# Optimization experiments

Hardware: AMD Instinct MI355X
Metric: run time of the kernel (lower is better)

## Reference

```python
import jax, jax.numpy as jnp
import numpy as np

DIM = 256
NUM_HEADS = 4
WINDOW = 64
EPS = 1e-6


def setup_inputs() -> dict:
    key = jax.random.key(0)
    ks = jax.random.split(key, 12)
    d = DIM
    s = 0.02
    return {
        "x": jax.random.normal(ks[0], (4, 2049, d), dtype=jnp.float32),
        "norm1_w": jnp.ones((d,), jnp.float32),
        "in_proj_w": jax.random.normal(ks[1], (3 * d, d), jnp.float32) * s,
        "in_proj_b": jnp.zeros((3 * d,), jnp.float32),
        "out_proj_w": jax.random.normal(ks[2], (d, d), jnp.float32) * s,
        "out_proj_b": jnp.zeros((d,), jnp.float32),
        "norm2_w": jnp.ones((d,), jnp.float32),
        "w1": jax.random.normal(ks[3], (2 * d, d), jnp.float32) * s,
        "b1": jnp.zeros((2 * d,), jnp.float32),
        "w2": jax.random.normal(ks[4], (d, 2 * d), jnp.float32) * s,
        "b2": jnp.zeros((d,), jnp.float32),
    }


def _rmsnorm(x, w):
    r = jax.lax.rsqrt(jnp.mean(x * x, axis=-1, keepdims=True) + EPS)
    return x * r * w


def _factorized_mask(size):
    # global token 0 attends/attended everywhere; others banded within WINDOW
    idx = jnp.arange(size)
    band = jnp.abs(idx[:, None] - idx[None, :]) <= WINDOW
    allowed = band | (idx[:, None] == 0) | (idx[None, :] == 0)
    return jnp.where(allowed, 0.0, -jnp.inf).astype(jnp.float32)


def reference(x, norm1_w, in_proj_w, in_proj_b, out_proj_w, out_proj_b,
              norm2_w, w1, b1, w2, b2):
    B, S, D = x.shape
    H = NUM_HEADS
    dh = D // H
    residual = x
    h = _rmsnorm(x, norm1_w)
    # fused qkv projection (torch MHA in_proj): [B,S,3D]
    qkv = h @ in_proj_w.T + in_proj_b
    q, k, v = jnp.split(qkv, 3, axis=-1)
    q = q.reshape(B, S, H, dh).transpose(0, 2, 1, 3)  # [B,H,S,dh]
    k = k.reshape(B, S, H, dh).transpose(0, 2, 1, 3)
    v = v.reshape(B, S, H, dh).transpose(0, 2, 1, 3)
    scores = jnp.einsum("bhqd,bhkd->bhqk", q, k) / jnp.sqrt(jnp.float32(dh))
    scores = scores + _factorized_mask(S)  # additive -inf mask
    attn = jax.nn.softmax(scores, axis=-1)
    ctx = jnp.einsum("bhqk,bhkd->bhqd", attn, v)
    ctx = ctx.transpose(0, 2, 1, 3).reshape(B, S, D)
    attn_out = ctx @ out_proj_w.T + out_proj_b
    x1 = residual + attn_out
    h2 = _rmsnorm(x1, norm2_w)
    ffn = jax.nn.gelu(h2 @ w1.T + b1, approximate=False) @ w2.T + b2
    return x1 + ffn
```

## Files before the change

kernel.cpp:

```cpp
#include <hip/hip_runtime.h>
#include <hip/hip_bf16.h>
#include <math.h>

#define BATCH 4
#define SEQ 2049
#define DIMD 256
#define WIN 64
#define M_ROWS (BATCH * SEQ)
#define M_PAD 8320

#define QBLK 33
#define NKB 10
#define PSTR 168
#define VGUARD 64
#define VW 2256
#define QKSTR 512

#define NSPLIT 33
#define VT_F4 288768

typedef __attribute__((ext_vector_type(8))) short short8;
typedef __attribute__((ext_vector_type(4))) float f32x4;
typedef __hip_bfloat16 bf16;

__device__ __forceinline__ float b2f(short u) {
    union { unsigned int i; float f; } c;
    c.i = ((unsigned int)(unsigned short)u) << 16;
    return c.f;
}
__device__ __forceinline__ short f2b(float f) {
    bf16 h = __float2bfloat16(f);
    return *reinterpret_cast<short*>(&h);
}

__global__ __launch_bounds__(256) void prep_kernel(
        const float* __restrict__ wq, const float* __restrict__ wo,
        const float* __restrict__ w1, const float* __restrict__ w2,
        bf16* __restrict__ oq, bf16* __restrict__ oo,
        bf16* __restrict__ o1, bf16* __restrict__ o2,
        const float* __restrict__ x, const float* __restrict__ nw,
        bf16* __restrict__ h, float4* __restrict__ vTz) {
    const int bi = blockIdx.x, tid = threadIdx.x;
    if (bi < 2048) {
        int i = bi * 256 + tid;
        if (i < 196608)      oq[i]          = __float2bfloat16(wq[i]);
        else if (i < 262144) oo[i - 196608] = __float2bfloat16(wo[i - 196608]);
        else if (i < 393216) o1[i - 262144] = __float2bfloat16(w1[i - 262144]);
        else                 o2[i - 393216] = __float2bfloat16(w2[i - 393216]);
        return;
    }
    if (bi >= 4097) {
        int zi = (bi - 4097) * 256 + tid;
        #pragma unroll
        for (int it = 0; it < 3; it++) {
            int idx = zi + it * 512 * 256;
            if (idx < VT_F4) vTz[idx] = (float4){0.f, 0.f, 0.f, 0.f};
        }
        return;
    }
    int wid = tid >> 6, lane = tid & 63;
    int row = (bi - 2048) * 4 + wid;
    if (row >= M_ROWS) return;
    const float4 v = reinterpret_cast<const float4*>(x + (size_t)row * DIMD)[lane];
    float ss = v.x * v.x + v.y * v.y + v.z * v.z + v.w * v.w;
    #pragma unroll
    for (int o = 1; o < 64; o <<= 1) ss += __shfl_xor(ss, o, 64);
    float r = rsqrtf(ss * (1.0f / DIMD) + 1e-6f);
    const float4 wv = reinterpret_cast<const float4*>(nw)[lane];
    bf16* hp = h + (size_t)row * DIMD + lane * 4;
    hp[0] = __float2bfloat16(v.x * r * wv.x);
    hp[1] = __float2bfloat16(v.y * r * wv.y);
    hp[2] = __float2bfloat16(v.z * r * wv.z);
    hp[3] = __float2bfloat16(v.w * r * wv.w);
}

__global__ __launch_bounds__(256) void gemm_qkv(
        const bf16* __restrict__ A, const bf16* __restrict__ B,
        const float* __restrict__ bias, bf16* __restrict__ qk, short* __restrict__ vT) {
    __shared__ __align__(16) short lA[8 * 128 * 8];
    __shared__ __align__(16) short lB[8 * 128 * 8];
    const int tid = threadIdx.x, lane = tid & 63, wid = tid >> 6;
    const int m0 = blockIdx.x * 128;
    const int n0 = blockIdx.y * 128;
    const int wr = wid >> 1, wc = wid & 1;
    const int r = lane & 15, g = lane >> 4;
    const int K = 256;

    f32x4 acc[4][4];
    #pragma unroll
    for (int i = 0; i < 4; i++)
        #pragma unroll
        for (int j = 0; j < 4; j++) acc[i][j] = (f32x4){0.f, 0.f, 0.f, 0.f};

    for (int k0 = 0; k0 < K; k0 += 64) {
        #pragma unroll
        for (int it = 0; it < 4; ++it) {
            int c = it * 256 + tid;
            int kc = c >> 7, row = c & 127;
            __builtin_amdgcn_global_load_lds(
                (const __attribute__((address_space(1))) void*)(A + (size_t)(m0 + row) * K + k0 + kc * 8),
                (__attribute__((address_space(3))) void*)&lA[c * 8], 16, 0, 0);
        }
        #pragma unroll
        for (int it = 0; it < 4; ++it) {
            int c = it * 256 + tid;
            int kc = c >> 7, row = c & 127;
            __builtin_amdgcn_global_load_lds(
                (const __attribute__((address_space(1))) void*)(B + (size_t)(n0 + row) * K + k0 + kc * 8),
                (__attribute__((address_space(3))) void*)&lB[c * 8], 16, 0, 0);
        }
        __syncthreads();
        #pragma unroll
        for (int kk = 0; kk < 2; kk++) {
            short8 a[4], b[4];
            #pragma unroll
            for (int mi = 0; mi < 4; mi++)
                a[mi] = *reinterpret_cast<const short8*>(&lA[((kk * 4 + g) * 128 + wr * 64 + mi * 16 + r) * 8]);
            #pragma unroll
            for (int ni = 0; ni < 4; ni++)
                b[ni] = *reinterpret_cast<const short8*>(&lB[((kk * 4 + g) * 128 + wc * 64 + ni * 16 + r) * 8]);
            #pragma unroll
            for (int mi = 0; mi < 4; mi++)
                #pragma unroll
                for (int ni = 0; ni < 4; ni++)
                    acc[mi][ni] = __builtin_amdgcn_mfma_f32_16x16x32_bf16(a[mi], b[ni], acc[mi][ni], 0, 0, 0);
        }
        __syncthreads();
    }

    const int c0 = lane & 15, r0 = (lane >> 4) * 4;
    const bool isV = (n0 >= 512);
    #pragma unroll
    for (int mi = 0; mi < 4; mi++) {
        #pragma unroll
        for (int ni = 0; ni < 4; ni++) {
            int col = n0 + wc * 64 + ni * 16 + c0;
            float bv = bias[col];
            #pragma unroll
            for (int j = 0; j < 4; j++) {
                int row = m0 + wr * 64 + mi * 16 + r0 + j;
                if (row < M_ROWS) {
                    float v = acc[mi][ni][j] + bv;
                    if (!isV) {
                        qk[(size_t)row * QKSTR + col] = __float2bfloat16(v);
                    } else {
                        int dcol = col - 512, hh = dcol >> 6, d = dcol & 63;
                        int bb = row >> 11;
                        int js = row - bb * SEQ;
                        if (js < 0) { bb--; js += SEQ; }
                        vT[((size_t)((bb * 4 + hh) * 64 + d)) * VW + VGUARD + js] = f2b(v);
                    }
                }
            }
        }
    }
}

template<int MODE, int BN>
__global__ __launch_bounds__(256) void gemm_lds(
        const bf16* __restrict__ A, const bf16* __restrict__ B,
        const float* __restrict__ bias, const float* __restrict__ resid,
        void* __restrict__ C, int M, int N, int K) {
    constexpr int FN = BN / 32;
    __shared__ __align__(16) short lA[8 * 128 * 8];
    __shared__ __align__(16) short lB[8 * BN * 8];
    const int tid = threadIdx.x, lane = tid & 63, wid = tid >> 6;
    const int m0 = blockIdx.x * 128;
    const int n0 = blockIdx.y * BN;
    const int wr = wid >> 1, wc = wid & 1;
    const int r = lane & 15, g = lane >> 4;

    f32x4 acc[4][FN];
    #pragma unroll
    for (int i = 0; i < 4; i++)
        #pragma unroll
        for (int j = 0; j < FN; j++) acc[i][j] = (f32x4){0.f, 0.f, 0.f, 0.f};

    for (int k0 = 0; k0 < K; k0 += 64) {
        #pragma unroll
        for (int it = 0; it < 4; ++it) {
            int c = it * 256 + tid;
            int kc = c >> 7, row = c & 127;
            __builtin_amdgcn_global_load_lds(
                (const __attribute__((address_space(1))) void*)(A + (size_t)(m0 + row) * K + k0 + kc * 8),
                (__attribute__((address_space(3))) void*)&lA[c * 8], 16, 0, 0);
        }
        #pragma unroll
        for (int it = 0; it < BN / 32; ++it) {
            int c = it * 256 + tid;
            int kc = c / BN, row = c % BN;
            __builtin_amdgcn_global_load_lds(
                (const __attribute__((address_space(1))) void*)(B + (size_t)(n0 + row) * K + k0 + kc * 8),
                (__attribute__((address_space(3))) void*)&lB[c * 8], 16, 0, 0);
        }
        __syncthreads();
        #pragma unroll
        for (int kk = 0; kk < 2; kk++) {
            short8 a[4], b[FN];
            #pragma unroll
            for (int mi = 0; mi < 4; mi++)
                a[mi] = *reinterpret_cast<const short8*>(&lA[((kk * 4 + g) * 128 + wr * 64 + mi * 16 + r) * 8]);
            #pragma unroll
            for (int ni = 0; ni < FN; ni++)
                b[ni] = *reinterpret_cast<const short8*>(&lB[((kk * 4 + g) * BN + wc * (BN / 2) + ni * 16 + r) * 8]);
            #pragma unroll
            for (int mi = 0; mi < 4; mi++)
                #pragma unroll
                for (int ni = 0; ni < FN; ni++)
                    acc[mi][ni] = __builtin_amdgcn_mfma_f32_16x16x32_bf16(a[mi], b[ni], acc[mi][ni], 0, 0, 0);
        }
        __syncthreads();
    }

    const int c0 = lane & 15, r0 = (lane >> 4) * 4;
    #pragma unroll
    for (int mi = 0; mi < 4; mi++) {
        #pragma unroll
        for (int ni = 0; ni < FN; ni++) {
            int col = n0 + wc * (BN / 2) + ni * 16 + c0;
            float bv = bias[col];
            #pragma unroll
            for (int j = 0; j < 4; j++) {
                int row = m0 + wr * 64 + mi * 16 + r0 + j;
                if (row < M) {
                    float v = acc[mi][ni][j] + bv;
                    if (MODE == 2) v = 0.5f * v * (1.0f + erff(v * 0.70710678118654752f));
                    if (MODE == 1) {
                        v += resid[(size_t)row * N + col];
                        reinterpret_cast<float*>(C)[(size_t)row * N + col] = v;
                    } else {
                        reinterpret_cast<bf16*>(C)[(size_t)row * N + col] = __float2bfloat16(v);
                    }
                }
            }
        }
    }
}

__global__ __launch_bounds__(256) void gemm_or(
        const bf16* __restrict__ A, const bf16* __restrict__ B,
        const float* __restrict__ bias, const float* __restrict__ resid,
        const float* __restrict__ nw,
        float* __restrict__ x1, bf16* __restrict__ h2) {
    __shared__ __align__(16) short lA[8 * 32 * 8];
    __shared__ __align__(16) short lB[8 * 256 * 8];
    __shared__ float osq[4][32];
    const int tid = threadIdx.x, lane = tid & 63, wid = tid >> 6;
    const int m0 = blockIdx.x * 32;
    const int wc = wid;
    const int r = lane & 15, g = lane >> 4;
    const int K = 256;

    f32x4 acc[2][4];
    #pragma unroll
    for (int i = 0; i < 2; i++)
        #pragma unroll
        for (int j = 0; j < 4; j++) acc[i][j] = (f32x4){0.f, 0.f, 0.f, 0.f};

    for (int k0 = 0; k0 < K; k0 += 64) {
        {
            int c = tid;
            int kc = c >> 5, row = c & 31;
            __builtin_amdgcn_global_load_lds(
                (const __attribute__((address_space(1))) void*)(A + (size_t)(m0 + row) * K + k0 + kc * 8),
                (__attribute__((address_space(3))) void*)&lA[c * 8], 16, 0, 0);
        }
        #pragma unroll
        for (int it = 0; it < 8; ++it) {
            int c = it * 256 + tid;
            int kc = c >> 8, row = c & 255;
            __builtin_amdgcn_global_load_lds(
                (const __attribute__((address_space(1))) void*)(B + (size_t)row * K + k0 + kc * 8),
                (__attribute__((address_space(3))) void*)&lB[c * 8], 16, 0, 0);
        }
        __syncthreads();
        #pragma unroll
        for (int kk = 0; kk < 2; kk++) {
            short8 a[2], b[4];
            #pragma unroll
            for (int mi = 0; mi < 2; mi++)
                a[mi] = *reinterpret_cast<const short8*>(&lA[((kk * 4 + g) * 32 + mi * 16 + r) * 8]);
            #pragma unroll
            for (int ni = 0; ni < 4; ni++)
                b[ni] = *reinterpret_cast<const short8*>(&lB[((kk * 4 + g) * 256 + wc * 64 + ni * 16 + r) * 8]);
            #pragma unroll
            for (int mi = 0; mi < 2; mi++)
                #pragma unroll
                for (int ni = 0; ni < 4; ni++)
                    acc[mi][ni] = __builtin_amdgcn_mfma_f32_16x16x32_bf16(a[mi], b[ni], acc[mi][ni], 0, 0, 0);
        }
        __syncthreads();
    }

    const int c0 = lane & 15, r0 = (lane >> 4) * 4;
    float ssq[2][4];
    #pragma unroll
    for (int mi = 0; mi < 2; mi++) {
        #pragma unroll
        for (int j = 0; j < 4; j++) {
            int row = m0 + mi * 16 + r0 + j;
            float s = 0.f;
            if (row < M_ROWS) {
                #pragma unroll
                for (int ni = 0; ni < 4; ni++) {
                    int col = wc * 64 + ni * 16 + c0;
                    float v = acc[mi][ni][j] + bias[col] + resid[(size_t)row * 256 + col];
                    acc[mi][ni][j] = v;
                    x1[(size_t)row * 256 + col] = v;
                    s += v * v;
                }
            }
            ssq[mi][j] = s;
        }
    }
    #pragma unroll
    for (int o = 1; o < 16; o <<= 1) {
        #pragma unroll
        for (int mi = 0; mi < 2; mi++)
            #pragma unroll
            for (int j = 0; j < 4; j++) ssq[mi][j] += __shfl_xor(ssq[mi][j], o, 64);
    }
    if (c0 == 0) {
        #pragma unroll
        for (int mi = 0; mi < 2; mi++)
            #pragma unroll
            for (int j = 0; j < 4; j++) osq[wc][mi * 16 + r0 + j] = ssq[mi][j];
    }
    __syncthreads();
    #pragma unroll
    for (int mi = 0; mi < 2; mi++) {
        #pragma unroll
        for (int j = 0; j < 4; j++) {
            int lr = mi * 16 + r0 + j;
            int row = m0 + lr;
            if (row < M_ROWS) {
                float tot = osq[0][lr] + osq[1][lr] + osq[2][lr] + osq[3][lr];
                float rs = rsqrtf(tot * (1.0f / 256.0f) + 1e-6f);
                #pragma unroll
                for (int ni = 0; ni < 4; ni++) {
                    int col = wc * 64 + ni * 16 + c0;
                    h2[(size_t)row * 256 + col] = __float2bfloat16(acc[mi][ni][j] * rs * nw[col]);
                }
            }
        }
    }
}

__global__ __launch_bounds__(256) void attn_partial(const bf16* __restrict__ qk,
                                                    const short* __restrict__ vT,
                                                    float* __restrict__ part) {
    __shared__ float q_s[64];
    __shared__ float p_s[64];
    __shared__ float meta[2];
    __shared__ float osum[4][64];
    const int tid = threadIdx.x;
    const int bh = blockIdx.x / NSPLIT, s = blockIdx.x % NSPLIT;
    const int b = bh >> 2, h = bh & 3;
    const size_t base = (size_t)b * SEQ;
    const int j0 = s * 64;
    const int lane = tid & 63, wid = tid >> 6;

    if (tid < 64) q_s[tid] = __bfloat162float(qk[base * QKSTR + h * 64 + tid]);
    __syncthreads();

    if (wid == 0) {
        int j = j0 + lane;
        float sc = -1e30f;
        if (j < SEQ) {
            const short8* kp = reinterpret_cast<const short8*>(
                reinterpret_cast<const short*>(qk) + (base + j) * QKSTR + 256 + h * 64);
            float acc = 0.f;
            #pragma unroll
            for (int d8 = 0; d8 < 8; ++d8) {
                short8 kv = kp[d8];
                #pragma unroll
                for (int e = 0; e < 8; ++e) acc += q_s[d8 * 8 + e] * b2f(kv[e]);
            }
            sc = acc * 0.125f;
        }
        float mx = sc;
        #pragma unroll
        for (int o = 1; o < 64; o <<= 1) mx = fmaxf(mx, __shfl_xor(mx, o, 64));
        float p = (j < SEQ) ? expf(sc - mx) : 0.f;
        p_s[lane] = p;
        float l = p;
        #pragma unroll
        for (int o = 1; o < 64; o <<= 1) l += __shfl_xor(l, o, 64);
        if (lane == 0) { meta[0] = mx; meta[1] = l; }
    }
    __syncthreads();

    const short* vrow = vT + ((size_t)bh * 64 + lane) * VW + VGUARD + j0;
    float oa = 0.f;
    #pragma unroll
    for (int i0 = 0; i0 < 16; i0++) {
        int i = wid + i0 * 4;
        if (j0 + i < SEQ) oa += p_s[i] * b2f(vrow[i]);
    }
    osum[wid][lane] = oa;
    __syncthreads();
    if (wid == 0) {
        float o = osum[0][lane] + osum[1][lane] + osum[2][lane] + osum[3][lane];
        float* pp = part + (size_t)(bh * NSPLIT + s) * 66;
        pp[lane] = o;
        if (lane == 0) { pp[64] = meta[0]; pp[65] = meta[1]; }
    }
}

__global__ __launch_bounds__(256) void attn_band_mfma(const bf16* __restrict__ qkb,
                                                      const short* __restrict__ vT,
                                                      const float* __restrict__ part,
                                                      short* __restrict__ ctx) {
    __shared__ short p_lds[4][16][PSTR];
    const short* qk = reinterpret_cast<const short*>(qkb);
    const int tid = threadIdx.x, lane = tid & 63, wid = tid >> 6;
    const int qb = blockIdx.x % QBLK;
    const int bh = blockIdx.x / QBLK;
    const int b = bh >> 2, h = bh & 3;
    const size_t rbase = (size_t)b * SEQ;
    const int q0w = qb * 64 + wid * 16;
    const int jbase = q0w - 64;
    const int lrow = lane & 15;
    const int koff = (lane >> 4) * 8;
    const int c0 = lrow, r0 = (lane >> 4) * 4;

    int qrow = q0w + lrow; if (qrow > SEQ - 1) qrow = SEQ - 1;
    const short* qp = qk + (rbase + qrow) * QKSTR + h * 64;
    short8 aq0 = *reinterpret_cast<const short8*>(qp + koff);
    short8 aq1 = *reinterpret_cast<const short8*>(qp + 32 + koff);

    const short* k0p = qk + rbase * QKSTR + 256 + h * 64;
    short8 k0a = *reinterpret_cast<const short8*>(k0p + koff);
    short8 k0b = *reinterpret_cast<const short8*>(k0p + 32 + koff);
    float s0 = 0.f;
    #pragma unroll
    for (int e = 0; e < 8; e++)
        s0 += b2f(aq0[e]) * b2f(k0a[e]) + b2f(aq1[e]) * b2f(k0b[e]);
    s0 += __shfl_xor(s0, 16, 64);
    s0 += __shfl_xor(s0, 32, 64);

    f32x4 s[NKB];
    #pragma unroll
    for (int n = 0; n < NKB; n++) {
        int j = jbase + n * 16 + lrow;
        int jc = j < 0 ? 0 : (j > SEQ - 1 ? SEQ - 1 : j);
        const short* kp = qk + (rbase + jc) * QKSTR + 256 + h * 64;
        short8 bk0 = *reinterpret_cast<const short8*>(kp + koff);
        short8 bk1 = *reinterpret_cast<const short8*>(kp + 32 + koff);
        f32x4 acc = (f32x4){0.f, 0.f, 0.f, 0.f};
        acc = __builtin_amdgcn_mfma_f32_16x16x32_bf16(aq0, bk0, acc, 0, 0, 0);
        acc = __builtin_amdgcn_mfma_f32_16x16x32_bf16(aq1, bk1, acc, 0, 0, 0);
        s[n] = acc;
    }

    const float SC = 0.125f * 1.44269504088896340736f;
    const bool g1 = (jbase > 0);
    float s0q[4], m4[4];
    #pragma unroll
    for (int jj = 0; jj < 4; jj++) {
        s0q[jj] = __shfl(s0, r0 + jj, 64) * SC;
        m4[jj] = g1 ? s0q[jj] : -1e30f;
    }
    #pragma unroll
    for (int n = 0; n < NKB; n++) {
        int j = jbase + n * 16 + c0;
        bool jv = (j >= 0) && (j < SEQ);
        #pragma unroll
        for (int jj = 0; jj < 4; jj++) {
            int q = q0w + r0 + jj;
            int dd = q - j; if (dd < 0) dd = -dd;
            bool allowed = jv && (dd <= WIN || j == 0);
            float v = allowed ? s[n][jj] * SC : -1e30f;
            s[n][jj] = v;
            m4[jj] = fmaxf(m4[jj], v);
        }
    }
    #pragma unroll
    for (int o = 1; o < 16; o <<= 1) {
        #pragma unroll
        for (int jj = 0; jj < 4; jj++) m4[jj] = fmaxf(m4[jj], __shfl_xor(m4[jj], o, 64));
    }

    float p0[4], l4[4];
    #pragma unroll
    for (int jj = 0; jj < 4; jj++) {
        p0[jj] = g1 ? exp2f(s0q[jj] - m4[jj]) : 0.f;
        l4[jj] = p0[jj];
    }
    #pragma unroll
    for (int n = 0; n < NKB; n++) {
        #pragma unroll
        for (int jj = 0; jj < 4; jj++) {
            float p = exp2f(s[n][jj] - m4[jj]);
            l4[jj] += p;
            p_lds[wid][r0 + jj][n * 16 + c0] = f2b(p);
        }
    }
    #pragma unroll
    for (int o = 1; o < 16; o <<= 1) {
        #pragma unroll
        for (int jj = 0; jj < 4; jj++) l4[jj] += __shfl_xor(l4[jj], o, 64);
    }

    __syncthreads();

    f32x4 o[4];
    #pragma unroll
    for (int dn = 0; dn < 4; dn++) o[dn] = (f32x4){0.f, 0.f, 0.f, 0.f};
    #pragma unroll
    for (int ks = 0; ks < NKB / 2; ks++) {
        short8 ap = *reinterpret_cast<const short8*>(&p_lds[wid][lrow][ks * 32 + koff]);
        int cc = VGUARD + jbase + ks * 32 + koff;
        #pragma unroll
        for (int dn = 0; dn < 4; dn++) {
            short8 bv = *reinterpret_cast<const short8*>(
                vT + ((size_t)bh * 64 + dn * 16 + lrow) * VW + cc);
            o[dn] = __builtin_amdgcn_mfma_f32_16x16x32_bf16(ap, bv, o[dn], 0, 0, 0);
        }
    }

    #pragma unroll
    for (int jj = 0; jj < 4; jj++) {
        int q = q0w + r0 + jj;
        if (q >= 1 && q < SEQ) {
            float rl = 1.0f / l4[jj];
            #pragma unroll
            for (int dn = 0; dn < 4; dn++) {
                float v0 = b2f(vT[((size_t)bh * 64 + dn * 16 + c0) * VW + VGUARD]);
                float val = (o[dn][jj] + p0[jj] * v0) * rl;
                ctx[(rbase + q) * 256 + h * 64 + dn * 16 + c0] = f2b(val);
            }
        }
    }

    if (qb == 0) {
        __syncthreads();
        if (wid == 0) {
            float m = (lane < NSPLIT) ? part[(size_t)(bh * NSPLIT + lane) * 66 + 64] : -1e30f;
            #pragma unroll
            for (int o2 = 1; o2 < 64; o2 <<= 1) m = fmaxf(m, __shfl_xor(m, o2, 64));
            float L = 0.f, ov = 0.f;
            for (int sp = 0; sp < NSPLIT; sp++) {
                const float* pp = part + (size_t)(bh * NSPLIT + sp) * 66;
                float w = expf(pp[64] - m);
                L += pp[65] * w;
                ov += pp[lane] * w;
            }
            ctx[rbase * 256 + h * 64 + lane] = f2b(ov / L);
        }
    }
}

extern "C" void kernel_launch(void* const* d_in, const int* in_sizes, int n_in,
                              void* d_out, int out_size, void* d_ws, size_t ws_size,
                              hipStream_t stream) {
    const float* x         = (const float*)d_in[0];
    const float* norm1_w   = (const float*)d_in[1];
    const float* in_proj_w = (const float*)d_in[2];
    const float* in_proj_b = (const float*)d_in[3];
    const float* out_proj_w= (const float*)d_in[4];
    const float* out_proj_b= (const float*)d_in[5];
    const float* norm2_w   = (const float*)d_in[6];
    const float* w1        = (const float*)d_in[7];
    const float* b1        = (const float*)d_in[8];
    const float* w2        = (const float*)d_in[9];
    const float* b2        = (const float*)d_in[10];
    float* out = (float*)d_out;

    const int M = M_ROWS;
    char* ws = (char*)d_ws;
    size_t off = 0;
    auto take = [&](size_t bytes) {
        char* p = ws + off;
        off = (off + bytes + 255) & ~(size_t)255;
        return p;
    };
    bf16* h_bf   = (bf16*)take((size_t)M_PAD * 256 * 2);
    bf16* qk_bf  = (bf16*)take((size_t)M_PAD * QKSTR * 2);
    bf16* ctx_bf = (bf16*)take((size_t)M_PAD * 256 * 2);
    float* x1    = (float*)take((size_t)M_PAD * 256 * 4);
    bf16* h2_bf  = (bf16*)take((size_t)M_PAD * 256 * 2);
    bf16* g_bf   = (bf16*)take((size_t)M_PAD * 512 * 2);
    bf16* wq_bf  = (bf16*)take(768 * 256 * 2);
    bf16* wo_bf  = (bf16*)take(256 * 256 * 2);
    bf16* w1_bf  = (bf16*)take(512 * 256 * 2);
    bf16* w2_bf  = (bf16*)take(256 * 512 * 2);
    float* part  = (float*)take((size_t)16 * NSPLIT * 66 * 4);
    short* vT    = (short*)take((size_t)16 * 64 * VW * 2);
    (void)ws_size; (void)in_sizes; (void)n_in; (void)out_size;

    prep_kernel<<<dim3(4609), dim3(256), 0, stream>>>(
        in_proj_w, out_proj_w, w1, w2, wq_bf, wo_bf, w1_bf, w2_bf,
        x, norm1_w, h_bf, (float4*)vT);
    gemm_qkv<<<dim3(65, 6), dim3(256), 0, stream>>>(h_bf, wq_bf, in_proj_b, qk_bf, vT);
    attn_partial<<<dim3(16 * NSPLIT), dim3(256), 0, stream>>>(qk_bf, vT, part);
    attn_band_mfma<<<dim3(16 * QBLK), dim3(256), 0, stream>>>(qk_bf, vT, part, (short*)ctx_bf);
    gemm_or<<<dim3(257), dim3(256), 0, stream>>>(ctx_bf, wo_bf, out_proj_b, x, norm2_w, x1, h2_bf);
    gemm_lds<2, 128><<<dim3(65, 4), dim3(256), 0, stream>>>(h2_bf, w1_bf, b1, (const float*)nullptr,
                                                            (void*)g_bf, M, 512, 256);
    gemm_lds<1, 64><<<dim3(65, 4), dim3(256), 0, stream>>>(g_bf, w2_bf, b2, x1,
                                                           (void*)out, M, 256, 512);
}
```

Measured before the change: 127.8 us.

## Fuse attention with out-projection/RMSNorm and fuse both FFN GEMMs

Attention is restructured so each block covers 16 query rows for all 4 heads of one batch. Each block keeps its context tile in LDS and immediately applies the out-projection, residual add and RMSNorm, so the ctx buffer and the separate gemm_or launch go away. The two FFN GEMMs are fused into one kernel that computes the GELU hidden activations in 128-column chunks in LDS and accumulates the second GEMM directly, which removes the g buffer round trip and a launch. In exchange, weight fragments are read straight from global memory without LDS staging, and the attention grid becomes smaller (516 blocks), which may lower efficiency.

```diff
diff --git a/kernel.cpp b/kernel.cpp
--- a/kernel.cpp
+++ b/kernel.cpp
@@ -9,9 +9,11 @@
 #define M_ROWS (BATCH * SEQ)
 #define M_PAD 8320
 
-#define QBLK 33
+#define QT16 129
 #define NKB 10
 #define PSTR 168
+#define CSTR 264
+#define GSTR 136
 #define VGUARD 64
 #define VW 2256
 #define QKSTR 512
@@ -156,196 +158,6 @@
     }
 }
 
-template<int MODE, int BN>
-__global__ __launch_bounds__(256) void gemm_lds(
-        const bf16* __restrict__ A, const bf16* __restrict__ B,
-        const float* __restrict__ bias, const float* __restrict__ resid,
-        void* __restrict__ C, int M, int N, int K) {
-    constexpr int FN = BN / 32;
-    __shared__ __align__(16) short lA[8 * 128 * 8];
-    __shared__ __align__(16) short lB[8 * BN * 8];
-    const int tid = threadIdx.x, lane = tid & 63, wid = tid >> 6;
-    const int m0 = blockIdx.x * 128;
-    const int n0 = blockIdx.y * BN;
-    const int wr = wid >> 1, wc = wid & 1;
-    const int r = lane & 15, g = lane >> 4;
-
-    f32x4 acc[4][FN];
-    #pragma unroll
-    for (int i = 0; i < 4; i++)
-        #pragma unroll
-        for (int j = 0; j < FN; j++) acc[i][j] = (f32x4){0.f, 0.f, 0.f, 0.f};
-
-    for (int k0 = 0; k0 < K; k0 += 64) {
-        #pragma unroll
-        for (int it = 0; it < 4; ++it) {
-            int c = it * 256 + tid;
-            int kc = c >> 7, row = c & 127;
-            __builtin_amdgcn_global_load_lds(
-                (const __attribute__((address_space(1))) void*)(A + (size_t)(m0 + row) * K + k0 + kc * 8),
-                (__attribute__((address_space(3))) void*)&lA[c * 8], 16, 0, 0);
-        }
-        #pragma unroll
-        for (int it = 0; it < BN / 32; ++it) {
-            int c = it * 256 + tid;
-            int kc = c / BN, row = c % BN;
-            __builtin_amdgcn_global_load_lds(
-                (const __attribute__((address_space(1))) void*)(B + (size_t)(n0 + row) * K + k0 + kc * 8),
-                (__attribute__((address_space(3))) void*)&lB[c * 8], 16, 0, 0);
-        }
-        __syncthreads();
-        #pragma unroll
-        for (int kk = 0; kk < 2; kk++) {
-            short8 a[4], b[FN];
-            #pragma unroll
-            for (int mi = 0; mi < 4; mi++)
-                a[mi] = *reinterpret_cast<const short8*>(&lA[((kk * 4 + g) * 128 + wr * 64 + mi * 16 + r) * 8]);
-            #pragma unroll
-            for (int ni = 0; ni < FN; ni++)
-                b[ni] = *reinterpret_cast<const short8*>(&lB[((kk * 4 + g) * BN + wc * (BN / 2) + ni * 16 + r) * 8]);
-            #pragma unroll
-            for (int mi = 0; mi < 4; mi++)
-                #pragma unroll
-                for (int ni = 0; ni < FN; ni++)
-                    acc[mi][ni] = __builtin_amdgcn_mfma_f32_16x16x32_bf16(a[mi], b[ni], acc[mi][ni], 0, 0, 0);
-        }
-        __syncthreads();
-    }
-
-    const int c0 = lane & 15, r0 = (lane >> 4) * 4;
-    #pragma unroll
-    for (int mi = 0; mi < 4; mi++) {
-        #pragma unroll
-        for (int ni = 0; ni < FN; ni++) {
-            int col = n0 + wc * (BN / 2) + ni * 16 + c0;
-            float bv = bias[col];
-            #pragma unroll
-            for (int j = 0; j < 4; j++) {
-                int row = m0 + wr * 64 + mi * 16 + r0 + j;
-                if (row < M) {
-                    float v = acc[mi][ni][j] + bv;
-                    if (MODE == 2) v = 0.5f * v * (1.0f + erff(v * 0.70710678118654752f));
-                    if (MODE == 1) {
-                        v += resid[(size_t)row * N + col];
-                        reinterpret_cast<float*>(C)[(size_t)row * N + col] = v;
-                    } else {
-                        reinterpret_cast<bf16*>(C)[(size_t)row * N + col] = __float2bfloat16(v);
-                    }
-                }
-            }
-        }
-    }
-}
-
-__global__ __launch_bounds__(256) void gemm_or(
-        const bf16* __restrict__ A, const bf16* __restrict__ B,
-        const float* __restrict__ bias, const float* __restrict__ resid,
-        const float* __restrict__ nw,
-        float* __restrict__ x1, bf16* __restrict__ h2) {
-    __shared__ __align__(16) short lA[8 * 32 * 8];
-    __shared__ __align__(16) short lB[8 * 256 * 8];
-    __shared__ float osq[4][32];
-    const int tid = threadIdx.x, lane = tid & 63, wid = tid >> 6;
-    const int m0 = blockIdx.x * 32;
-    const int wc = wid;
-    const int r = lane & 15, g = lane >> 4;
-    const int K = 256;
-
-    f32x4 acc[2][4];
-    #pragma unroll
-    for (int i = 0; i < 2; i++)
-        #pragma unroll
-        for (int j = 0; j < 4; j++) acc[i][j] = (f32x4){0.f, 0.f, 0.f, 0.f};
-
-    for (int k0 = 0; k0 < K; k0 += 64) {
-        {
-            int c = tid;
-            int kc = c >> 5, row = c & 31;
-            __builtin_amdgcn_global_load_lds(
-                (const __attribute__((address_space(1))) void*)(A + (size_t)(m0 + row) * K + k0 + kc * 8),
-                (__attribute__((address_space(3))) void*)&lA[c * 8], 16, 0, 0);
-        }
-        #pragma unroll
-        for (int it = 0; it < 8; ++it) {
-            int c = it * 256 + tid;
-            int kc = c >> 8, row = c & 255;
-            __builtin_amdgcn_global_load_lds(
-                (const __attribute__((address_space(1))) void*)(B + (size_t)row * K + k0 + kc * 8),
-                (__attribute__((address_space(3))) void*)&lB[c * 8], 16, 0, 0);
-        }
-        __syncthreads();
-        #pragma unroll
-        for (int kk = 0; kk < 2; kk++) {
-            short8 a[2], b[4];
-            #pragma unroll
-            for (int mi = 0; mi < 2; mi++)
-                a[mi] = *reinterpret_cast<const short8*>(&lA[((kk * 4 + g) * 32 + mi * 16 + r) * 8]);
-            #pragma unroll
-            for (int ni = 0; ni < 4; ni++)
-                b[ni] = *reinterpret_cast<const short8*>(&lB[((kk * 4 + g) * 256 + wc * 64 + ni * 16 + r) * 8]);
-            #pragma unroll
-            for (int mi = 0; mi < 2; mi++)
-                #pragma unroll
-                for (int ni = 0; ni < 4; ni++)
-                    acc[mi][ni] = __builtin_amdgcn_mfma_f32_16x16x32_bf16(a[mi], b[ni], acc[mi][ni], 0, 0, 0);
-        }
-        __syncthreads();
-    }
-
-    const int c0 = lane & 15, r0 = (lane >> 4) * 4;
-    float ssq[2][4];
-    #pragma unroll
-    for (int mi = 0; mi < 2; mi++) {
-        #pragma unroll
-        for (int j = 0; j < 4; j++) {
-            int row = m0 + mi * 16 + r0 + j;
-            float s = 0.f;
-            if (row < M_ROWS) {
-                #pragma unroll
-                for (int ni = 0; ni < 4; ni++) {
-                    int col = wc * 64 + ni * 16 + c0;
-                    float v = acc[mi][ni][j] + bias[col] + resid[(size_t)row * 256 + col];
-                    acc[mi][ni][j] = v;
-                    x1[(size_t)row * 256 + col] = v;
-                    s += v * v;
-                }
-            }
-            ssq[mi][j] = s;
-        }
-    }
-    #pragma unroll
-    for (int o = 1; o < 16; o <<= 1) {
-        #pragma unroll
-        for (int mi = 0; mi < 2; mi++)
-            #pragma unroll
-            for (int j = 0; j < 4; j++) ssq[mi][j] += __shfl_xor(ssq[mi][j], o, 64);
-    }
-    if (c0 == 0) {
-        #pragma unroll
-        for (int mi = 0; mi < 2; mi++)
-            #pragma unroll
-            for (int j = 0; j < 4; j++) osq[wc][mi * 16 + r0 + j] = ssq[mi][j];
-    }
-    __syncthreads();
-    #pragma unroll
-    for (int mi = 0; mi < 2; mi++) {
-        #pragma unroll
-        for (int j = 0; j < 4; j++) {
-            int lr = mi * 16 + r0 + j;
-            int row = m0 + lr;
-            if (row < M_ROWS) {
-                float tot = osq[0][lr] + osq[1][lr] + osq[2][lr] + osq[3][lr];
-                float rs = rsqrtf(tot * (1.0f / 256.0f) + 1e-6f);
-                #pragma unroll
-                for (int ni = 0; ni < 4; ni++) {
-                    int col = wc * 64 + ni * 16 + c0;
-                    h2[(size_t)row * 256 + col] = __float2bfloat16(acc[mi][ni][j] * rs * nw[col]);
-                }
-            }
-        }
-    }
-}
-
 __global__ __launch_bounds__(256) void attn_partial(const bf16* __restrict__ qk,
                                                     const short* __restrict__ vT,
                                                     float* __restrict__ part) {
@@ -407,24 +219,27 @@
     }
 }
 
-__global__ __launch_bounds__(256) void attn_band_mfma(const bf16* __restrict__ qkb,
-                                                      const short* __restrict__ vT,
-                                                      const float* __restrict__ part,
-                                                      short* __restrict__ ctx) {
+__global__ __launch_bounds__(256) void attn_or(
+        const bf16* __restrict__ qkb, const short* __restrict__ vT,
+        const float* __restrict__ part, const bf16* __restrict__ wo,
+        const float* __restrict__ ob, const float* __restrict__ x,
+        const float* __restrict__ nw, float* __restrict__ x1, bf16* __restrict__ h2) {
     __shared__ short p_lds[4][16][PSTR];
+    __shared__ short ctx_lds[16][CSTR];
+    __shared__ float osq[4][16];
     const short* qk = reinterpret_cast<const short*>(qkb);
-    const int tid = threadIdx.x, lane = tid & 63, wid = tid >> 6;
-    const int qb = blockIdx.x % QBLK;
-    const int bh = blockIdx.x / QBLK;
-    const int b = bh >> 2, h = bh & 3;
+    const int tid = threadIdx.x, lane = tid & 63, h = tid >> 6;
+    const int qt = blockIdx.x % QT16;
+    const int b = blockIdx.x / QT16;
+    const int bh = b * 4 + h;
     const size_t rbase = (size_t)b * SEQ;
-    const int q0w = qb * 64 + wid * 16;
-    const int jbase = q0w - 64;
+    const int q0 = qt * 16;
+    const int jbase = q0 - 64;
     const int lrow = lane & 15;
     const int koff = (lane >> 4) * 8;
     const int c0 = lrow, r0 = (lane >> 4) * 4;
 
-    int qrow = q0w + lrow; if (qrow > SEQ - 1) qrow = SEQ - 1;
+    int qrow = q0 + lrow; if (qrow > SEQ - 1) qrow = SEQ - 1;
     const short* qp = qk + (rbase + qrow) * QKSTR + h * 64;
     short8 aq0 = *reinterpret_cast<const short8*>(qp + koff);
     short8 aq1 = *reinterpret_cast<const short8*>(qp + 32 + koff);
@@ -467,7 +282,7 @@
         bool jv = (j >= 0) && (j < SEQ);
         #pragma unroll
         for (int jj = 0; jj < 4; jj++) {
-            int q = q0w + r0 + jj;
+            int q = q0 + r0 + jj;
             int dd = q - j; if (dd < 0) dd = -dd;
             bool allowed = jv && (dd <= WIN || j == 0);
             float v = allowed ? s[n][jj] * SC : -1e30f;
@@ -493,7 +308,7 @@
         for (int jj = 0; jj < 4; jj++) {
             float p = exp2f(s[n][jj] - m4[jj]);
             l4[jj] += p;
-            p_lds[wid][r0 + jj][n * 16 + c0] = f2b(p);
+            p_lds[h][r0 + jj][n * 16 + c0] = f2b(p);
         }
     }
     #pragma unroll
@@ -502,14 +317,12 @@
         for (int jj = 0; jj < 4; jj++) l4[jj] += __shfl_xor(l4[jj], o, 64);
     }
 
-    __syncthreads();
-
     f32x4 o[4];
     #pragma unroll
     for (int dn = 0; dn < 4; dn++) o[dn] = (f32x4){0.f, 0.f, 0.f, 0.f};
     #pragma unroll
     for (int ks = 0; ks < NKB / 2; ks++) {
-        short8 ap = *reinterpret_cast<const short8*>(&p_lds[wid][lrow][ks * 32 + koff]);
+        short8 ap = *reinterpret_cast<const short8*>(&p_lds[h][lrow][ks * 32 + koff]);
         int cc = VGUARD + jbase + ks * 32 + koff;
         #pragma unroll
         for (int dn = 0; dn < 4; dn++) {
@@ -521,32 +334,182 @@
 
     #pragma unroll
     for (int jj = 0; jj < 4; jj++) {
-        int q = q0w + r0 + jj;
-        if (q >= 1 && q < SEQ) {
-            float rl = 1.0f / l4[jj];
-            #pragma unroll
-            for (int dn = 0; dn < 4; dn++) {
-                float v0 = b2f(vT[((size_t)bh * 64 + dn * 16 + c0) * VW + VGUARD]);
-                float val = (o[dn][jj] + p0[jj] * v0) * rl;
-                ctx[(rbase + q) * 256 + h * 64 + dn * 16 + c0] = f2b(val);
-            }
-        }
-    }
-
-    if (qb == 0) {
+        int q = q0 + r0 + jj;
+        int ql = r0 + jj;
+        float rl = 1.0f / l4[jj];
+        #pragma unroll
+        for (int dn = 0; dn < 4; dn++) {
+            float v0 = b2f(vT[((size_t)bh * 64 + dn * 16 + c0) * VW + VGUARD]);
+            float val = (o[dn][jj] + p0[jj] * v0) * rl;
+            if (q >= 1) ctx_lds[ql][h * 64 + dn * 16 + c0] = f2b(val);
+        }
+    }
+
+    if (qt == 0) {
+        float m = (lane < NSPLIT) ? part[(size_t)(bh * NSPLIT + lane) * 66 + 64] : -1e30f;
+        #pragma unroll
+        for (int o2 = 1; o2 < 64; o2 <<= 1) m = fmaxf(m, __shfl_xor(m, o2, 64));
+        float L = 0.f, ov = 0.f;
+        for (int sp = 0; sp < NSPLIT; sp++) {
+            const float* pp = part + (size_t)(bh * NSPLIT + sp) * 66;
+            float w = expf(pp[64] - m);
+            L += pp[65] * w;
+            ov += pp[lane] * w;
+        }
+        ctx_lds[0][h * 64 + lane] = f2b(ov / L);
+    }
+    __syncthreads();
+
+    f32x4 oacc[4];
+    #pragma unroll
+    for (int ni = 0; ni < 4; ni++) oacc[ni] = (f32x4){0.f, 0.f, 0.f, 0.f};
+    #pragma unroll
+    for (int ks = 0; ks < 8; ks++) {
+        short8 a = *reinterpret_cast<const short8*>(&ctx_lds[lrow][ks * 32 + koff]);
+        #pragma unroll
+        for (int ni = 0; ni < 4; ni++) {
+            short8 bfrag = *reinterpret_cast<const short8*>(
+                reinterpret_cast<const short*>(wo) + (size_t)(h * 64 + ni * 16 + lrow) * 256 + ks * 32 + koff);
+            oacc[ni] = __builtin_amdgcn_mfma_f32_16x16x32_bf16(a, bfrag, oacc[ni], 0, 0, 0);
+        }
+    }
+
+    float ssq[4];
+    #pragma unroll
+    for (int jj = 0; jj < 4; jj++) {
+        int row = q0 + r0 + jj;
+        float sq = 0.f;
+        if (row < SEQ) {
+            #pragma unroll
+            for (int ni = 0; ni < 4; ni++) {
+                int col = h * 64 + ni * 16 + c0;
+                float v = oacc[ni][jj] + ob[col] + x[(rbase + row) * 256 + col];
+                oacc[ni][jj] = v;
+                x1[(rbase + row) * 256 + col] = v;
+                sq += v * v;
+            }
+        }
+        ssq[jj] = sq;
+    }
+    #pragma unroll
+    for (int o2 = 1; o2 < 16; o2 <<= 1) {
+        #pragma unroll
+        for (int jj = 0; jj < 4; jj++) ssq[jj] += __shfl_xor(ssq[jj], o2, 64);
+    }
+    if (c0 == 0) {
+        #pragma unroll
+        for (int jj = 0; jj < 4; jj++) osq[h][r0 + jj] = ssq[jj];
+    }
+    __syncthreads();
+    #pragma unroll
+    for (int jj = 0; jj < 4; jj++) {
+        int lr = r0 + jj;
+        int row = q0 + lr;
+        if (row < SEQ) {
+            float tot = osq[0][lr] + osq[1][lr] + osq[2][lr] + osq[3][lr];
+            float rs = rsqrtf(tot * (1.0f / 256.0f) + 1e-6f);
+            #pragma unroll
+            for (int ni = 0; ni < 4; ni++) {
+                int col = h * 64 + ni * 16 + c0;
+                h2[(rbase + row) * 256 + col] = __float2bfloat16(oacc[ni][jj] * rs * nw[col]);
+            }
+        }
+    }
+}
+
+__global__ __launch_bounds__(256) void ffn_fused(
+        const bf16* __restrict__ h2, const bf16* __restrict__ w1b, const float* __restrict__ b1,
+        const bf16* __restrict__ w2b, const float* __restrict__ b2, const float* __restrict__ x1,
+        float* __restrict__ out) {
+    __shared__ short g_lds[32][GSTR];
+    const int tid = threadIdx.x, lane = tid & 63, wid = tid >> 6;
+    const int m0 = blockIdx.x * 32;
+    const int lrow = lane & 15;
+    const int koff = (lane >> 4) * 8;
+    const int c0 = lrow, r0 = (lane >> 4) * 4;
+
+    f32x4 oacc[2][4];
+    #pragma unroll
+    for (int mi = 0; mi < 2; mi++)
+        #pragma unroll
+        for (int ni = 0; ni < 4; ni++) oacc[mi][ni] = (f32x4){0.f, 0.f, 0.f, 0.f};
+
+    int ar[2];
+    #pragma unroll
+    for (int mi = 0; mi < 2; mi++) {
+        int rr = m0 + mi * 16 + lrow;
+        ar[mi] = rr < M_ROWS ? rr : M_ROWS - 1;
+    }
+
+    for (int ch = 0; ch < 4; ch++) {
+        f32x4 gacc[2][2];
+        #pragma unroll
+        for (int mi = 0; mi < 2; mi++)
+            #pragma unroll
+            for (int ni = 0; ni < 2; ni++) gacc[mi][ni] = (f32x4){0.f, 0.f, 0.f, 0.f};
+        #pragma unroll
+        for (int ks = 0; ks < 8; ks++) {
+            short8 a[2];
+            #pragma unroll
+            for (int mi = 0; mi < 2; mi++)
+                a[mi] = *reinterpret_cast<const short8*>(
+                    reinterpret_cast<const short*>(h2) + (size_t)ar[mi] * 256 + ks * 32 + koff);
+            #pragma unroll
+            for (int ni = 0; ni < 2; ni++) {
+                short8 bfrag = *reinterpret_cast<const short8*>(
+                    reinterpret_cast<const short*>(w1b) +
+                    (size_t)(ch * 128 + wid * 32 + ni * 16 + lrow) * 256 + ks * 32 + koff);
+                #pragma unroll
+                for (int mi = 0; mi < 2; mi++)
+                    gacc[mi][ni] = __builtin_amdgcn_mfma_f32_16x16x32_bf16(a[mi], bfrag, gacc[mi][ni], 0, 0, 0);
+            }
+        }
+        if (ch > 0) __syncthreads();
+        #pragma unroll
+        for (int mi = 0; mi < 2; mi++) {
+            #pragma unroll
+            for (int ni = 0; ni < 2; ni++) {
+                int colg = wid * 32 + ni * 16 + c0;
+                float bv = b1[ch * 128 + colg];
+                #pragma unroll
+                for (int jj = 0; jj < 4; jj++) {
+                    float v = gacc[mi][ni][jj] + bv;
+                    v = 0.5f * v * (1.0f + erff(v * 0.70710678118654752f));
+                    g_lds[mi * 16 + r0 + jj][colg] = f2b(v);
+                }
+            }
+        }
         __syncthreads();
-        if (wid == 0) {
-            float m = (lane < NSPLIT) ? part[(size_t)(bh * NSPLIT + lane) * 66 + 64] : -1e30f;
-            #pragma unroll
-            for (int o2 = 1; o2 < 64; o2 <<= 1) m = fmaxf(m, __shfl_xor(m, o2, 64));
-            float L = 0.f, ov = 0.f;
-            for (int sp = 0; sp < NSPLIT; sp++) {
-                const float* pp = part + (size_t)(bh * NSPLIT + sp) * 66;
-                float w = expf(pp[64] - m);
-                L += pp[65] * w;
-                ov += pp[lane] * w;
-            }
-            ctx[rbase * 256 + h * 64 + lane] = f2b(ov / L);
+        #pragma unroll
+        for (int k = 0; k < 4; k++) {
+            short8 ag[2];
+            #pragma unroll
+            for (int mi = 0; mi < 2; mi++)
+                ag[mi] = *reinterpret_cast<const short8*>(&g_lds[mi * 16 + lrow][k * 32 + koff]);
+            #pragma unroll
+            for (int ni = 0; ni < 4; ni++) {
+                short8 bfrag = *reinterpret_cast<const short8*>(
+                    reinterpret_cast<const short*>(w2b) +
+                    (size_t)(wid * 64 + ni * 16 + lrow) * 512 + ch * 128 + k * 32 + koff);
+                #pragma unroll
+                for (int mi = 0; mi < 2; mi++)
+                    oacc[mi][ni] = __builtin_amdgcn_mfma_f32_16x16x32_bf16(ag[mi], bfrag, oacc[mi][ni], 0, 0, 0);
+            }
+        }
+    }
+
+    #pragma unroll
+    for (int mi = 0; mi < 2; mi++) {
+        #pragma unroll
+        for (int ni = 0; ni < 4; ni++) {
+            int col = wid * 64 + ni * 16 + c0;
+            float bv = b2[col];
+            #pragma unroll
+            for (int jj = 0; jj < 4; jj++) {
+                int row = m0 + mi * 16 + r0 + jj;
+                if (row < M_ROWS)
+                    out[(size_t)row * 256 + col] = oacc[mi][ni][jj] + bv + x1[(size_t)row * 256 + col];
+            }
         }
     }
 }
@@ -567,7 +530,6 @@
     const float* b2        = (const float*)d_in[10];
     float* out = (float*)d_out;
 
-    const int M = M_ROWS;
     char* ws = (char*)d_ws;
     size_t off = 0;
     auto take = [&](size_t bytes) {
@@ -577,10 +539,8 @@
     };
     bf16* h_bf   = (bf16*)take((size_t)M_PAD * 256 * 2);
     bf16* qk_bf  = (bf16*)take((size_t)M_PAD * QKSTR * 2);
-    bf16* ctx_bf = (bf16*)take((size_t)M_PAD * 256 * 2);
     float* x1    = (float*)take((size_t)M_PAD * 256 * 4);
     bf16* h2_bf  = (bf16*)take((size_t)M_PAD * 256 * 2);
-    bf16* g_bf   = (bf16*)take((size_t)M_PAD * 512 * 2);
     bf16* wq_bf  = (bf16*)take(768 * 256 * 2);
     bf16* wo_bf  = (bf16*)take(256 * 256 * 2);
     bf16* w1_bf  = (bf16*)take(512 * 256 * 2);
@@ -594,10 +554,7 @@
         x, norm1_w, h_bf, (float4*)vT);
     gemm_qkv<<<dim3(65, 6), dim3(256), 0, stream>>>(h_bf, wq_bf, in_proj_b, qk_bf, vT);
     attn_partial<<<dim3(16 * NSPLIT), dim3(256), 0, stream>>>(qk_bf, vT, part);
-    attn_band_mfma<<<dim3(16 * QBLK), dim3(256), 0, stream>>>(qk_bf, vT, part, (short*)ctx_bf);
-    gemm_or<<<dim3(257), dim3(256), 0, stream>>>(ctx_bf, wo_bf, out_proj_b, x, norm2_w, x1, h2_bf);
-    gemm_lds<2, 128><<<dim3(65, 4), dim3(256), 0, stream>>>(h2_bf, w1_bf, b1, (const float*)nullptr,
-                                                            (void*)g_bf, M, 512, 256);
-    gemm_lds<1, 64><<<dim3(65, 4), dim3(256), 0, stream>>>(g_bf, w2_bf, b2, x1,
-                                                           (void*)out, M, 256, 512);
-}
+    attn_or<<<dim3(4 * QT16), dim3(256), 0, stream>>>(
+        qk_bf, vT, part, wo_bf, out_proj_b, x, norm2_w, x1, h2_bf);
+    ffn_fused<<<dim3(257), dim3(256), 0, stream>>>(h2_bf, w1_bf, b1, w2_bf, b2, x1, out);
+}
```

New measurement: 121.4 us. -5.0%, faster.
